# Kernel optimization log

Hardware: AMD Instinct MI355X
Metric: run time of the kernel (lower is better)

The kernel has to match this reference:

```python
import jax, jax.numpy as jnp
import numpy as np

N_NODES = 10000
N_EDGES = 160000
MUL = 128          # channel multiplicity
N_SPECIES = 10
SH_OFF = [0, 1, 4, 9, 16]   # spherical-harmonic offsets for l=0..3 (2l+1 each)
RADIAL_IN = 8
SIN_DIM = 32
MAX_DENSITY = 100.0


def setup_inputs() -> dict:
    key = jax.random.key(0)
    ks = jax.random.split(key, 16)
    inp = {
        'node_attrs': jax.random.normal(ks[0], (N_NODES, N_SPECIES), jnp.float32),
        'node_feats': jax.random.normal(ks[1], (N_NODES, MUL), jnp.float32),
        'edge_attrs': jax.random.normal(ks[2], (N_EDGES, 16), jnp.float32),
        'edge_feats': jax.random.normal(ks[3], (N_EDGES, RADIAL_IN), jnp.float32),
        'edge_index': jax.random.randint(ks[4], (2, N_EDGES), 0, N_NODES, jnp.int64),
        'W_up': jax.random.normal(ks[5], (MUL, MUL), jnp.float32),
        'Wr1': jax.random.normal(ks[6], (RADIAL_IN, 64), jnp.float32),
        'Wr2': jax.random.normal(ks[7], (64, 64), jnp.float32),
        'Wr3': jax.random.normal(ks[8], (64, 64), jnp.float32),
        'Wr4': jax.random.normal(ks[9], (64, 4 * MUL), jnp.float32),
        'Wd': jax.random.normal(ks[10], (RADIAL_IN, 1), jnp.float32),
        'Wsin': jax.random.normal(ks[11], (SIN_DIM, MUL), jnp.float32),
        'Wlin': jax.random.normal(ks[12], (4, MUL, MUL), jnp.float32),
        'Wskip': jax.random.normal(ks[13], (4, MUL, N_SPECIES, MUL), jnp.float32),
    }
    return inp


def _sinusoidal_embedding(x):
    # continuous sinusoidal embedding: dim=32, max_density=100
    half = SIN_DIM // 2
    freqs = jnp.exp(-jnp.log(MAX_DENSITY) * jnp.arange(half, dtype=x.dtype) / half)
    ang = x[:, None] * freqs[None, :]          # [N, 16]
    return jnp.concatenate([jnp.sin(ang), jnp.cos(ang)], axis=-1)  # [N, 32]


def reference(node_attrs, node_feats, edge_attrs, edge_feats, edge_index,
              W_up, Wr1, Wr2, Wr3, Wr4, Wd, Wsin, Wlin, Wskip):
    N = node_feats.shape[0]
    sender, receiver = edge_index[0], edge_index[1]

    # linear_up (e3nn o3.Linear on 128x0e, fan-in normalized)
    x = node_feats @ (W_up / np.float32(np.sqrt(MUL)))          # [N, 128]

    # radial MLP: FullyConnectedNet([8,64,64,64,512], silu), fan-in normalized
    h = edge_feats
    for W in (Wr1, Wr2, Wr3):
        h = jax.nn.silu(h @ (W / np.float32(np.sqrt(W.shape[0]))))
    tp_w = (h @ (Wr4 / np.float32(np.sqrt(64)))).reshape(-1, 4, MUL)  # [E, 4, 128]

    # equivariant TP: scalar node feats (x) gathered by sender, uvu path per SH l
    xs = x[sender]                                              # [E, 128]
    weighted = xs[:, None, :] * tp_w                            # [E, 4, 128]
    blocks = []
    for l in range(4):
        sh_l = edge_attrs[:, SH_OFF[l]:SH_OFF[l + 1]]           # [E, 2l+1]
        blk = weighted[:, l, :, None] * sh_l[:, None, :]        # [E, 128, 2l+1]
        blocks.append(blk.reshape(blk.shape[0], -1))
    mji = jnp.concatenate(blocks, axis=-1)                      # [E, 2048]

    # per-edge density gate
    density = jnp.tanh((edge_feats @ Wd) ** 2)                  # [E, 1]

    # scatter-sum messages and density to receivers
    message = jax.ops.segment_sum(mji, receiver, num_segments=N)        # [N, 2048]
    rho = jax.ops.segment_sum(density, receiver, num_segments=N)       # [N, 1]
    message = message / (rho + 1.0)

    # density embedding injected into the l=0 block
    demb = _sinusoidal_embedding(rho[:, 0]) @ Wsin              # [N, 128]
    message = message.at[:, :MUL].add(demb)

    # per-l linear (irreps_mid -> irreps_out), skip_tp with node_attrs, reshape
    out_blocks = []
    for l in range(4):
        d = 2 * l + 1
        blk = message[:, MUL * SH_OFF[l]:MUL * SH_OFF[l + 1]].reshape(N, MUL, d)
        blk = jnp.einsum('nuk,uv->nvk', blk, Wlin[l]) / np.float32(np.sqrt(MUL))
        blk = jnp.einsum('nvk,na,vaw->nwk', blk, node_attrs, Wskip[l]) \
              / np.float32(np.sqrt(MUL * N_SPECIES))
        out_blocks.append(blk)
    return jnp.concatenate(out_blocks, axis=-1)                 # [N, 128, 16]
```

## Files before the change

### kernel.cpp

```cpp
#include <hip/hip_runtime.h>
#include <hip/hip_bf16.h>

#define N_NODES 10000
#define N_EDGES 160000

typedef _Float16 h8 __attribute__((ext_vector_type(8)));
typedef _Float16 h4 __attribute__((ext_vector_type(4)));
typedef float f32x4 __attribute__((ext_vector_type(4)));

__device__ __forceinline__ float silu_f(float v){ return v / (1.f + expf(-v)); }

__global__ __launch_bounds__(256) void k_pre(const float* __restrict__ Wr2,
                                             const float* __restrict__ Wr3,
                                             const float* __restrict__ Wr4,
                                             const float* __restrict__ Wup,
                                             const float* __restrict__ Wlin,
                                             const float* __restrict__ Wskip,
                                             const int* __restrict__ eidx,
                                             _Float16* __restrict__ Wr2T,
                                             _Float16* __restrict__ Wr3T,
                                             _Float16* __restrict__ Wr4T,
                                             _Float16* __restrict__ WupT,
                                             _Float16* __restrict__ WC16T,
                                             int* __restrict__ cnt){
  const int b = blockIdx.x;
  __shared__ float wl[128];
  if (b < 224){
    const int idx = b*256 + threadIdx.x;
    if (idx < 4096){
      const int n = idx >> 6, k = idx & 63;
      Wr2T[idx] = (_Float16)(Wr2[k*64 + n] * 0.125f);
    } else if (idx < 8192){
      const int j = idx - 4096;
      const int n = j >> 6, k = j & 63;
      Wr3T[j] = (_Float16)(Wr3[k*64 + n] * 0.125f);
    } else if (idx < 40960){
      const int j = idx - 8192;
      const int n = j >> 6, k = j & 63;
      Wr4T[j] = (_Float16)(Wr4[k*512 + n] * 0.125f);
    } else if (idx < 57344){
      const int j = idx - 40960;
      const int u = j >> 7, k = j & 127;
      WupT[j] = (_Float16)(Wup[k*128 + u] * 0.08838834764831843f);
    }
  } else if (b < 736){
    const int lu = b - 224;
    const int l  = lu >> 7, u = lu & 127;
    if (threadIdx.x < 128) wl[threadIdx.x] = Wlin[lu*128 + threadIdx.x];
    __syncthreads();
    const float* Wsk = Wskip + (size_t)l * 163840;
    for (int i = threadIdx.x; i < 1280; i += 256){
      float acc = 0.f;
      #pragma unroll 16
      for (int v = 0; v < 128; ++v) acc += wl[v] * Wsk[v*1280 + i];
      const int a = i >> 7, w = i & 127;
      WC16T[((size_t)l*128 + w)*1280 + a*128 + u] =
          (_Float16)(acc * 0.0024705294220065465f);
    }
  } else {
    const int e = (b - 736)*256 + threadIdx.x;
    if (e < N_EDGES) atomicAdd(&cnt[eidx[N_EDGES + e]], 1);
  }
}

__global__ __launch_bounds__(256) void k_scan(const int* __restrict__ cnt,
                                              int* __restrict__ off,
                                              int* __restrict__ cur){
  __shared__ int sums[256];
  const int t = threadIdx.x;
  const int base = t * 40;
  int s = 0;
  for (int i = 0; i < 40; ++i){
    const int idx = base + i;
    if (idx < N_NODES) s += cnt[idx];
  }
  sums[t] = s;
  __syncthreads();
  for (int st = 1; st < 256; st <<= 1){
    const int v = (t >= st) ? sums[t - st] : 0;
    __syncthreads();
    sums[t] += v;
    __syncthreads();
  }
  int pre = (t > 0) ? sums[t - 1] : 0;
  for (int i = 0; i < 40; ++i){
    const int idx = base + i;
    if (idx < N_NODES){
      off[idx] = pre; cur[idx] = pre;
      pre += cnt[idx];
    }
  }
  if (t == 255) off[N_NODES] = sums[255];
}

__global__ __launch_bounds__(256) void k_mid(const int* __restrict__ eidx,
                                             int* __restrict__ cur,
                                             int* __restrict__ elist,
                                             int* __restrict__ esnd,
                                             const float* __restrict__ nf,
                                             const _Float16* __restrict__ WupT,
                                             float* __restrict__ x){
  const int b = blockIdx.x;
  const int tid = threadIdx.x;
  alignas(16) __shared__ _Float16 s_nf[64*128];
  alignas(16) __shared__ _Float16 s_wt[128*128];

  if (b < 625){
    const int e = b * 256 + tid;
    if (e < N_EDGES){
      const int pos = atomicAdd(&cur[eidx[N_EDGES + e]], 1);
      elist[pos] = e;
      esnd[pos]  = eidx[e];
    }
    return;
  }

  const int n0 = (b - 625) * 64;
  {
    const int rl = tid >> 2, part = tid & 3;
    const int gr = n0 + rl;
    #pragma unroll
    for (int j = 0; j < 4; ++j){
      const int cu = part*4 + j;
      h8 hv = (h8){};
      if (gr < N_NODES){
        const float4 v0 = *(const float4*)(nf + (size_t)gr*128 + cu*8);
        const float4 v1 = *(const float4*)(nf + (size_t)gr*128 + cu*8 + 4);
        hv[0]=(_Float16)v0.x; hv[1]=(_Float16)v0.y; hv[2]=(_Float16)v0.z; hv[3]=(_Float16)v0.w;
        hv[4]=(_Float16)v1.x; hv[5]=(_Float16)v1.y; hv[6]=(_Float16)v1.z; hv[7]=(_Float16)v1.w;
      }
      const int cs = (cu & 8) | ((cu & 7) ^ (rl & 7));
      *(h8*)&s_nf[rl*128 + cs*8] = hv;
    }
  }
  {
    const int rl = tid >> 1, part = tid & 1;
    #pragma unroll
    for (int j = 0; j < 8; ++j){
      const int cu = part*8 + j;
      const h8 v = *(const h8*)&WupT[(size_t)rl*128 + cu*8];
      const int cs = (cu & 8) | ((cu & 7) ^ (rl & 7));
      *(h8*)&s_wt[rl*128 + cs*8] = v;
    }
  }
  __syncthreads();

  const int wid = tid >> 6, lane = tid & 63;
  const int li = lane & 15, kg = lane >> 4;

  f32x4 acc[8];
  #pragma unroll
  for (int i = 0; i < 8; ++i) acc[i] = (f32x4){0,0,0,0};

  const int row = wid*16 + li;
  #pragma unroll
  for (int s = 0; s < 4; ++s){
    const int ca = s*4 + kg;
    const int csA = (ca & 8) | ((ca & 7) ^ (row & 7));
    const h8 af = *(const h8*)&s_nf[row*128 + csA*8];
    #pragma unroll
    for (int nt = 0; nt < 8; ++nt){
      const int u = nt*16 + li;
      const int csB = (ca & 8) | ((ca & 7) ^ (u & 7));
      const h8 bf = *(const h8*)&s_wt[u*128 + csB*8];
      acc[nt] = __builtin_amdgcn_mfma_f32_16x16x32_f16(af, bf, acc[nt], 0, 0, 0);
    }
  }
  #pragma unroll
  for (int nt = 0; nt < 8; ++nt){
    #pragma unroll
    for (int r = 0; r < 4; ++r){
      const int gr = n0 + wid*16 + kg*4 + r;
      if (gr < N_NODES) x[(size_t)gr*128 + nt*16 + li] = acc[nt][r];
    }
  }
}

__global__ __launch_bounds__(256) void k_fused(const float* __restrict__ ef,
                                               const float* __restrict__ ea,
                                               const float* __restrict__ x,
                                               const float* __restrict__ Wr1,
                                               const float* __restrict__ Wd,
                                               const _Float16* __restrict__ Wr2T,
                                               const _Float16* __restrict__ Wr3T,
                                               const _Float16* __restrict__ Wr4T,
                                               const float* __restrict__ Wsin,
                                               const int* __restrict__ off,
                                               const int* __restrict__ elist,
                                               const int* __restrict__ esnd,
                                               float* __restrict__ msg){
  const int n0 = blockIdx.x * 4;
  const int tid = threadIdx.x;
  const int lane = tid & 63, wid = tid >> 6;
  const int li = lane & 15, kg = lane >> 4;
  const int u = tid & 127, h = tid >> 7;

  __shared__ int   s_eid[32];
  __shared__ float s_ef[32][8];
  __shared__ float s_w1[8][64];
  alignas(16) __shared__ _Float16 s_xs[32][136];
  alignas(16) __shared__ _Float16 s_actA[32][64];
  alignas(16) __shared__ _Float16 s_actB[32][64];
  alignas(16) __shared__ _Float16 s_w2[32][520];
  alignas(16) __shared__ float s_sh[32][16];
  __shared__ float s_dd[32];
  __shared__ float s_rho[4];
  __shared__ int   s_offs[5];
  __shared__ float s_emb[4][32];

  if (tid < 5) s_offs[tid] = off[n0 + tid];
  if (tid < 4) s_rho[tid] = 0.f;
  for (int j = tid; j < 512; j += 256) s_w1[j >> 6][j & 63] = Wr1[j];
  __syncthreads();

  const int beg = s_offs[0], end = s_offs[4];
  const int ngrp = (end - beg + 31) >> 5;

  float a0[8] = {0,0,0,0,0,0,0,0};
  float a1[8] = {0,0,0,0,0,0,0,0};
  float a2[8] = {0,0,0,0,0,0,0,0};
  float a3[8] = {0,0,0,0,0,0,0,0};

  for (int grp = 0; grp < ngrp; ++grp){
    const int pbase = beg + grp*32;

    if (tid < 32) s_eid[tid] = (pbase + tid < end) ? elist[pbase + tid] : -1;
    __syncthreads();

    {
      const int e = tid >> 3, i = tid & 7;
      const int eid = s_eid[e];
      s_ef[e][i] = (eid >= 0) ? ef[(size_t)eid*8 + i] : 0.f;
    }
    {
      const int e = tid >> 3, qq = tid & 7;
      const int p = pbase + e;
      const int snd = (p < end) ? esnd[p] : 0;
      const float4* xp = (const float4*)(x + (size_t)snd*128 + qq*16);
      #pragma unroll
      for (int j = 0; j < 4; ++j){
        const float4 v = xp[j];
        h4 hv; hv[0]=(_Float16)v.x; hv[1]=(_Float16)v.y; hv[2]=(_Float16)v.z; hv[3]=(_Float16)v.w;
        *(h4*)&s_xs[e][qq*16 + j*4] = hv;
      }
    }
    #pragma unroll
    for (int c2 = 0; c2 < 2; ++c2){
      const int idx = c2*256 + tid;
      const int slot = idx >> 4, jj = idx & 15;
      const int eid = s_eid[slot];
      s_sh[slot][jj] = (eid >= 0) ? ea[(size_t)eid*16 + jj] : 0.f;
    }
    __syncthreads();

    if (tid < 32){
      float s = 0.f;
      #pragma unroll
      for (int i = 0; i < 8; ++i) s += s_ef[tid][i] * Wd[i];
      s_dd[tid] = tanhf(s*s);
    }

    {
      const int e = tid >> 3, ng = tid & 7;
      float hv[8] = {0,0,0,0,0,0,0,0};
      #pragma unroll
      for (int k = 0; k < 8; ++k){
        const float ev = s_ef[e][k] * 0.3535533905932738f;
        #pragma unroll
        for (int j = 0; j < 8; ++j) hv[j] += ev * s_w1[k][ng*8 + j];
      }
      h8 o;
      #pragma unroll
      for (int j = 0; j < 8; ++j) o[j] = (_Float16)silu_f(hv[j]);
      *(h8*)&s_actA[e][(ng ^ (e & 7))*8] = o;
    }
    __syncthreads();

    {
      h8 af[2];
      #pragma unroll
      for (int s = 0; s < 2; ++s)
        af[s] = *(const h8*)&Wr2T[(size_t)(wid*16 + li)*64 + s*32 + kg*8];
      #pragma unroll
      for (int nt = 0; nt < 2; ++nt){
        const int e = nt*16 + li;
        f32x4 acc = (f32x4){0,0,0,0};
        #pragma unroll
        for (int s = 0; s < 2; ++s){
          const h8 bf = *(const h8*)&s_actA[e][((s*4 + kg) ^ (e & 7))*8];
          acc = __builtin_amdgcn_mfma_f32_16x16x32_f16(af[s], bf, acc, 0, 0, 0);
        }
        #pragma unroll
        for (int r = 0; r < 4; ++r){
          const int n = wid*16 + kg*4 + r;
          s_actB[e][((n >> 3) ^ (e & 7))*8 + (n & 7)] = (_Float16)silu_f(acc[r]);
        }
      }
    }
    __syncthreads();

    {
      h8 af[2];
      #pragma unroll
      for (int s = 0; s < 2; ++s)
        af[s] = *(const h8*)&Wr3T[(size_t)(wid*16 + li)*64 + s*32 + kg*8];
      #pragma unroll
      for (int nt = 0; nt < 2; ++nt){
        const int e = nt*16 + li;
        f32x4 acc = (f32x4){0,0,0,0};
        #pragma unroll
        for (int s = 0; s < 2; ++s){
          const h8 bf = *(const h8*)&s_actB[e][((s*4 + kg) ^ (e & 7))*8];
          acc = __builtin_amdgcn_mfma_f32_16x16x32_f16(af[s], bf, acc, 0, 0, 0);
        }
        #pragma unroll
        for (int r = 0; r < 4; ++r){
          const int n = wid*16 + kg*4 + r;
          s_actA[e][((n >> 3) ^ (e & 7))*8 + (n & 7)] = (_Float16)silu_f(acc[r]);
        }
      }
    }
    __syncthreads();

    {
      h8 bf[2][2];
      #pragma unroll
      for (int nt = 0; nt < 2; ++nt){
        const int e = nt*16 + li;
        #pragma unroll
        for (int s = 0; s < 2; ++s)
          bf[nt][s] = *(const h8*)&s_actA[e][((s*4 + kg) ^ (e & 7))*8];
      }
      #pragma unroll
      for (int p = 0; p < 2; ++p){
        #pragma unroll
        for (int mt = 0; mt < 4; ++mt){
          const int nbase = wid*128 + p*64 + mt*16;
          h8 af[2];
          #pragma unroll
          for (int s = 0; s < 2; ++s)
            af[s] = *(const h8*)&Wr4T[(size_t)(nbase + li)*64 + s*32 + kg*8];
          f32x4 acc[2];
          #pragma unroll
          for (int nt = 0; nt < 2; ++nt){
            acc[nt] = (f32x4){0,0,0,0};
            #pragma unroll
            for (int s = 0; s < 2; ++s)
              acc[nt] = __builtin_amdgcn_mfma_f32_16x16x32_f16(af[s], bf[nt][s], acc[nt], 0, 0, 0);
          }
          const int c0 = nbase + kg*4;
          const int u0 = c0 & 127;
          #pragma unroll
          for (int nt = 0; nt < 2; ++nt){
            const int e = nt*16 + li;
            const h4 xv = *(const h4*)&s_xs[e][u0];
            h4 ov;
            #pragma unroll
            for (int r = 0; r < 4; ++r) ov[r] = (_Float16)acc[nt][r] * xv[r];
            *(h4*)&s_w2[e][c0] = ov;
          }
        }
      }
    }
    __syncthreads();

    int lo0 = s_offs[0] - pbase; lo0 = lo0 < 0 ? 0 : lo0;
    int hi0 = s_offs[1] - pbase; hi0 = hi0 > 32 ? 32 : (hi0 < 0 ? 0 : hi0);
    int lo1 = s_offs[1] - pbase; lo1 = lo1 < 0 ? 0 : lo1;
    int hi1 = s_offs[2] - pbase; hi1 = hi1 > 32 ? 32 : (hi1 < 0 ? 0 : hi1);
    int lo2 = s_offs[2] - pbase; lo2 = lo2 < 0 ? 0 : lo2;
    int hi2 = s_offs[3] - pbase; hi2 = hi2 > 32 ? 32 : (hi2 < 0 ? 0 : hi2);
    int lo3 = s_offs[3] - pbase; lo3 = lo3 < 0 ? 0 : lo3;
    int hi3 = s_offs[4] - pbase; hi3 = hi3 > 32 ? 32 : (hi3 < 0 ? 0 : hi3);

#define ACC_H0(A, LO, HI)                                            \
    for (int s = (LO); s < (HI); ++s){                               \
      const float wa  = (float)s_w2[s][u];                           \
      const float wb  = (float)s_w2[s][128 + u];                     \
      const float wcv = (float)s_w2[s][256 + u];                     \
      const float4 sa = *(const float4*)&s_sh[s][0];                 \
      const float4 sb = *(const float4*)&s_sh[s][4];                 \
      A[0] += wa*sa.x;                                               \
      A[1] += wb*sa.y;  A[2] += wb*sa.z;  A[3] += wb*sa.w;           \
      A[4] += wcv*sb.x; A[5] += wcv*sb.y;                            \
      A[6] += wcv*sb.z; A[7] += wcv*sb.w;                            \
    }
#define ACC_H1(A, LO, HI)                                            \
    for (int s = (LO); s < (HI); ++s){                               \
      const float wcv = (float)s_w2[s][256 + u];                     \
      const float wd  = (float)s_w2[s][384 + u];                     \
      const float4 sa = *(const float4*)&s_sh[s][8];                 \
      const float4 sb = *(const float4*)&s_sh[s][12];                \
      A[0] += wcv*sa.x;                                              \
      A[1] += wd*sa.y;  A[2] += wd*sa.z;  A[3] += wd*sa.w;           \
      A[4] += wd*sb.x;  A[5] += wd*sb.y;                             \
      A[6] += wd*sb.z;  A[7] += wd*sb.w;                             \
    }

    if (h == 0){
      ACC_H0(a0, lo0, hi0) ACC_H0(a1, lo1, hi1)
      ACC_H0(a2, lo2, hi2) ACC_H0(a3, lo3, hi3)
    } else {
      ACC_H1(a0, lo0, hi0) ACC_H1(a1, lo1, hi1)
      ACC_H1(a2, lo2, hi2) ACC_H1(a3, lo3, hi3)
    }

    if (tid < 4){
      int lo = s_offs[tid]     - pbase; lo = lo < 0 ? 0 : lo;
      int hi = s_offs[tid + 1] - pbase; hi = hi > 32 ? 32 : (hi < 0 ? 0 : hi);
      float r = 0.f;
      for (int s = lo; s < hi; ++s) r += s_dd[s];
      s_rho[tid] += r;
    }
    __syncthreads();
  }

  if (tid < 64){
    const int ni = tid >> 4, f = tid & 15;
    const float fr  = expf(-0.28782313662425572f * (float)f);
    const float ang = s_rho[ni] * fr;
    s_emb[ni][f]      = sinf(ang);
    s_emb[ni][f + 16] = cosf(ang);
  }
  __syncthreads();

  float db0 = 0.f, db1 = 0.f, db2 = 0.f, db3 = 0.f;
  if (h == 0){
    #pragma unroll 8
    for (int j = 0; j < 32; ++j){
      const float wsv = Wsin[j*128 + u];
      db0 += s_emb[0][j]*wsv; db1 += s_emb[1][j]*wsv;
      db2 += s_emb[2][j]*wsv; db3 += s_emb[3][j]*wsv;
    }
  }
  const float t0 = 1.f/(s_rho[0]+1.f), t1 = 1.f/(s_rho[1]+1.f);
  const float t2 = 1.f/(s_rho[2]+1.f), t3 = 1.f/(s_rho[3]+1.f);
  #pragma unroll
  for (int j = 0; j < 8; ++j){
    float v0 = a0[j]*t0, v1 = a1[j]*t1, v2 = a2[j]*t2, v3 = a3[j]*t3;
    if (h == 0 && j == 0){ v0 += db0; v1 += db1; v2 += db2; v3 += db3; }
    const size_t base = (size_t)(h*8 + j)*128 + u;
    msg[(size_t)(n0+0)*2048 + base] = v0;
    msg[(size_t)(n0+1)*2048 + base] = v1;
    msg[(size_t)(n0+2)*2048 + base] = v2;
    msg[(size_t)(n0+3)*2048 + base] = v3;
  }
}

template<int L, int D>
__device__ __forceinline__ void final_body(const int bb,
                                           const float* __restrict__ msg,
                                           const float* __restrict__ attrs,
                                           const _Float16* __restrict__ WC16T,
                                           float* __restrict__ outD,
                                           _Float16* __restrict__ sA,
                                           _Float16* __restrict__ sB,
                                           _Float16* __restrict__ sAttr){
  constexpr int OFF  = (L==0 ? 0 : L==1 ? 1 : L==2 ? 4 : 9);
  constexpr int ROWS = N_NODES * D;
  const int r0  = bb * 128;
  const int tid = threadIdx.x;

  {
    const int rl = tid >> 2, quarter = tid & 3;
    const int gr = r0 + rl;
    h8 vals[4];
    if (gr < ROWS){
      const int n = gr / D, k = gr - n*D;
      const float4* src = (const float4*)(msg + (size_t)n*2048 + (size_t)(OFF+k)*128 + quarter*32);
      #pragma unroll
      for (int j = 0; j < 4; ++j){
        const float4 v0 = src[j*2], v1 = src[j*2+1];
        h8 hv;
        hv[0]=(_Float16)v0.x; hv[1]=(_Float16)v0.y; hv[2]=(_Float16)v0.z; hv[3]=(_Float16)v0.w;
        hv[4]=(_Float16)v1.x; hv[5]=(_Float16)v1.y; hv[6]=(_Float16)v1.z; hv[7]=(_Float16)v1.w;
        vals[j] = hv;
      }
    } else {
      #pragma unroll
      for (int j = 0; j < 4; ++j) vals[j] = (h8){};
    }
    #pragma unroll
    for (int j = 0; j < 4; ++j){
      const int cu = quarter*4 + j;
      const int cs = (cu & 8) | ((cu & 7) ^ (rl & 7));
      *(h8*)&sA[rl*128 + cs*8] = vals[j];
    }
  }
  for (int i = tid; i < 1280; i += 512){
    const int rl = i / 10, aa = i - rl*10;
    const int gr = r0 + rl;
    sAttr[i] = (gr < ROWS) ? (_Float16)attrs[(gr / D)*10 + aa] : (_Float16)0.f;
  }
  {
    const int w = tid >> 2, part = tid & 3;
    const _Float16* src = WC16T + ((size_t)L*128 + w)*1280 + part*16;
    #pragma unroll
    for (int j = 0; j < 2; ++j){
      const h8 v = *(const h8*)(src + j*8);
      const int cc = part*2 + j;
      *(h8*)&sB[w*64 + (cc ^ (w & 7))*8] = v;
    }
  }
  __syncthreads();

  const int wid = tid >> 6, lane = tid & 63;
  const int wm = wid >> 2, wn = wid & 3;
  const int li = lane & 15, kg = lane >> 4;

  f32x4 acc[4][2];
  #pragma unroll
  for (int m = 0; m < 4; ++m)
    #pragma unroll
    for (int nn = 0; nn < 2; ++nn) acc[m][nn] = (f32x4){0,0,0,0};

  for (int step = 0; step < 20; ++step){
    _Float16* sbc = (step & 1) ? (sB + 8192) : sB;
    _Float16* sbn = (step & 1) ? sB : (sB + 8192);
    const bool more = (step + 1 < 20);
    h8 pre[2];
    if (more){
      const int a2 = (step+1) >> 1, u02 = ((step+1) & 1) << 6;
      const _Float16* src = WC16T + ((size_t)L*128 + (tid>>2))*1280 + a2*128 + u02 + (tid&3)*16;
      #pragma unroll
      for (int j = 0; j < 2; ++j) pre[j] = *(const h8*)(src + j*8);
    }

    const int a  = step >> 1;
    const int uh = (step & 1) << 3;

    h8 afr[4][2], bfr[2][2];
    #pragma unroll
    for (int m = 0; m < 4; ++m){
      const int row = wm*64 + m*16 + li;
      const _Float16 av = sAttr[row*10 + a];
      h8 avx;
      #pragma unroll
      for (int j = 0; j < 8; ++j) avx[j] = av;
      #pragma unroll
      for (int s = 0; s < 2; ++s){
        const int ca = uh + s*4 + kg;
        const int cs = (ca & 8) | ((ca & 7) ^ (row & 7));
        const h8 mA = *(const h8*)&sA[row*128 + cs*8];
        afr[m][s] = mA * avx;
      }
    }
    #pragma unroll
    for (int nn = 0; nn < 2; ++nn){
      const int w = wn*32 + nn*16 + li;
      #pragma unroll
      for (int s = 0; s < 2; ++s){
        const int cb = s*4 + kg;
        bfr[nn][s] = *(const h8*)&sbc[w*64 + ((cb ^ (w & 7)))*8];
      }
    }
    #pragma unroll
    for (int s = 0; s < 2; ++s)
      #pragma unroll
      for (int m = 0; m < 4; ++m)
        #pragma unroll
        for (int nn = 0; nn < 2; ++nn)
          acc[m][nn] = __builtin_amdgcn_mfma_f32_16x16x32_f16(afr[m][s], bfr[nn][s], acc[m][nn], 0, 0, 0);

    if (more){
      const int w = tid >> 2, part = tid & 3;
      #pragma unroll
      for (int j = 0; j < 2; ++j){
        const int cc = part*2 + j;
        *(h8*)&sbn[w*64 + (cc ^ (w & 7))*8] = pre[j];
      }
    }
    __syncthreads();
  }

  #pragma unroll
  for (int m = 0; m < 4; ++m){
    const int rbase = r0 + wm*64 + m*16 + kg*4;
    #pragma unroll
    for (int rr = 0; rr < 4; ++rr){
      const int gr = rbase + rr;
      if (gr < ROWS){
        float* op = outD + (size_t)gr*128;
        #pragma unroll
        for (int nn = 0; nn < 2; ++nn)
          op[wn*32 + nn*16 + li] = acc[m][nn][rr];
      }
    }
  }
}

__global__ __launch_bounds__(512) void k_final_all(const float* __restrict__ msg,
                                                   const float* __restrict__ attrs,
                                                   const _Float16* __restrict__ WC16T,
                                                   float* __restrict__ outD){
  alignas(16) __shared__ _Float16 sA[128*128];
  alignas(16) __shared__ _Float16 sB[2*64*128];
  __shared__ _Float16 sAttr[128*10];
  const int b = blockIdx.x;
  if (b < 79)       final_body<0,1>(b,       msg, attrs, WC16T, outD,            sA, sB, sAttr);
  else if (b < 314) final_body<1,3>(b - 79,  msg, attrs, WC16T, outD + 1280000,  sA, sB, sAttr);
  else if (b < 705) final_body<2,5>(b - 314, msg, attrs, WC16T, outD + 5120000,  sA, sB, sAttr);
  else              final_body<3,7>(b - 705, msg, attrs, WC16T, outD + 11520000, sA, sB, sAttr);
}

__global__ __launch_bounds__(256) void k_merge(const float* __restrict__ outD,
                                               float* __restrict__ out){
  const int n0 = blockIdx.x * 4;
  const int tid = threadIdx.x;
  __shared__ float lds[4*16*132];

  {
    const float4* src = (const float4*)(outD + (size_t)n0*128);
    for (int j = tid; j < 128; j += 256){
      const int row = j >> 5, c4 = j & 31;
      *(float4*)&lds[(row*16 + 0)*132 + c4*4] = src[j];
    }
  }
  {
    const float4* src = (const float4*)(outD + 1280000 + (size_t)n0*3*128);
    for (int j = tid; j < 384; j += 256){
      const int row = j >> 5, c4 = j & 31;
      const int nloc = row/3, k = row - nloc*3;
      *(float4*)&lds[(nloc*16 + 1 + k)*132 + c4*4] = src[j];
    }
  }
  {
    const float4* src = (const float4*)(outD + 5120000 + (size_t)n0*5*128);
    for (int j = tid; j < 640; j += 256){
      const int row = j >> 5, c4 = j & 31;
      const int nloc = row/5, k = row - nloc*5;
      *(float4*)&lds[(nloc*16 + 4 + k)*132 + c4*4] = src[j];
    }
  }
  {
    const float4* src = (const float4*)(outD + 11520000 + (size_t)n0*7*128);
    for (int j = tid; j < 896; j += 256){
      const int row = j >> 5, c4 = j & 31;
      const int nloc = row/7, k = row - nloc*7;
      *(float4*)&lds[(nloc*16 + 9 + k)*132 + c4*4] = src[j];
    }
  }
  __syncthreads();

  for (int j = tid; j < 2048; j += 256){
    const int nloc = j >> 9, qv = j & 511;
    const int w = qv >> 2, s0 = (qv & 3) << 2;
    float4 v;
    v.x = lds[(nloc*16 + s0 + 0)*132 + w];
    v.y = lds[(nloc*16 + s0 + 1)*132 + w];
    v.z = lds[(nloc*16 + s0 + 2)*132 + w];
    v.w = lds[(nloc*16 + s0 + 3)*132 + w];
    *(float4*)&out[(size_t)(n0 + nloc)*2048 + qv*4] = v;
  }
}

extern "C" void kernel_launch(void* const* d_in, const int* in_sizes, int n_in,
                              void* d_out, int out_size, void* d_ws, size_t ws_size,
                              hipStream_t stream){
  const float* node_attrs = (const float*)d_in[0];
  const float* node_feats = (const float*)d_in[1];
  const float* edge_attrs = (const float*)d_in[2];
  const float* edge_feats = (const float*)d_in[3];
  const int*   edge_index = (const int*)d_in[4];
  const float* W_up  = (const float*)d_in[5];
  const float* Wr1   = (const float*)d_in[6];
  const float* Wr2   = (const float*)d_in[7];
  const float* Wr3   = (const float*)d_in[8];
  const float* Wr4   = (const float*)d_in[9];
  const float* Wd    = (const float*)d_in[10];
  const float* Wsin  = (const float*)d_in[11];
  const float* Wlin  = (const float*)d_in[12];
  const float* Wskip = (const float*)d_in[13];
  float* out = (float*)d_out;

  float* outD    = (float*)d_ws;
  float* msg     = outD + 20480000;
  float* x       = msg + 20480000;
  _Float16* WC16T= (_Float16*)(x + 1280000);
  int* cnt   = (int*)(WC16T + 655360);
  int* off   = cnt + 10000;
  int* cur   = off + 10016;
  int* elist = cur + 10000;
  int* esnd  = elist + 160000;
  _Float16* Wr2T = (_Float16*)(esnd + 160000);
  _Float16* Wr3T = Wr2T + 4096;
  _Float16* Wr4T = Wr3T + 4096;
  _Float16* WupT = Wr4T + 32768;

  hipMemsetAsync(cnt, 0, (size_t)10000 * sizeof(int), stream);

  k_pre<<<1361, 256, 0, stream>>>(Wr2, Wr3, Wr4, W_up, Wlin, Wskip, edge_index,
                                  Wr2T, Wr3T, Wr4T, WupT, WC16T, cnt);
  k_scan<<<1, 256, 0, stream>>>(cnt, off, cur);
  k_mid<<<782, 256, 0, stream>>>(edge_index, cur, elist, esnd,
                                 node_feats, WupT, x);

  k_fused<<<N_NODES/4, 256, 0, stream>>>(edge_feats, edge_attrs, x,
                                         Wr1, Wd, Wr2T, Wr3T, Wr4T, Wsin,
                                         off, elist, esnd, msg);

  k_final_all<<<1252, 512, 0, stream>>>(msg, node_attrs, WC16T, outD);

  k_merge<<<2500, 256, 0, stream>>>(outD, out);
}
```

Baseline: 335.6 us.

## Store messages in fp16, fuse final per-l GEMMs with output merge, split Wr4 pass

The fused edge kernel now builds the Wr4 weights in two passes over a half-width LDS buffer and accumulates between them, which shrinks shared memory per block. It writes the message as fp16 instead of fp32. A new final kernel processes 16 nodes per block across all four l blocks. It writes output directly in the interleaved [N,128,16] layout, so the separate per-l output buffer and merge kernel are gone. This removes an fp32 round trip through global memory and one launch, but adds an extra barrier per edge group and keeps the message at fp16 precision.

```diff
diff --git a/kernel.cpp b/kernel.cpp
--- a/kernel.cpp
+++ b/kernel.cpp
@@ -188,7 +188,7 @@
                                                const int* __restrict__ off,
                                                const int* __restrict__ elist,
                                                const int* __restrict__ esnd,
-                                               float* __restrict__ msg){
+                                               _Float16* __restrict__ msg16){
   const int n0 = blockIdx.x * 4;
   const int tid = threadIdx.x;
   const int lane = tid & 63, wid = tid >> 6;
@@ -198,10 +198,10 @@
   __shared__ int   s_eid[32];
   __shared__ float s_ef[32][8];
   __shared__ float s_w1[8][64];
-  alignas(16) __shared__ _Float16 s_xs[32][136];
+  alignas(16) __shared__ _Float16 s_xs[32][132];
   alignas(16) __shared__ _Float16 s_actA[32][64];
   alignas(16) __shared__ _Float16 s_actB[32][64];
-  alignas(16) __shared__ _Float16 s_w2[32][520];
+  alignas(16) __shared__ _Float16 s_w2[32][264];
   alignas(16) __shared__ float s_sh[32][16];
   __shared__ float s_dd[32];
   __shared__ float s_rho[4];
@@ -317,48 +317,6 @@
         for (int r = 0; r < 4; ++r){
           const int n = wid*16 + kg*4 + r;
           s_actA[e][((n >> 3) ^ (e & 7))*8 + (n & 7)] = (_Float16)silu_f(acc[r]);
-        }
-      }
-    }
-    __syncthreads();
-
-    {
-      h8 bf[2][2];
-      #pragma unroll
-      for (int nt = 0; nt < 2; ++nt){
-        const int e = nt*16 + li;
-        #pragma unroll
-        for (int s = 0; s < 2; ++s)
-          bf[nt][s] = *(const h8*)&s_actA[e][((s*4 + kg) ^ (e & 7))*8];
-      }
-      #pragma unroll
-      for (int p = 0; p < 2; ++p){
-        #pragma unroll
-        for (int mt = 0; mt < 4; ++mt){
-          const int nbase = wid*128 + p*64 + mt*16;
-          h8 af[2];
-          #pragma unroll
-          for (int s = 0; s < 2; ++s)
-            af[s] = *(const h8*)&Wr4T[(size_t)(nbase + li)*64 + s*32 + kg*8];
-          f32x4 acc[2];
-          #pragma unroll
-          for (int nt = 0; nt < 2; ++nt){
-            acc[nt] = (f32x4){0,0,0,0};
-            #pragma unroll
-            for (int s = 0; s < 2; ++s)
-              acc[nt] = __builtin_amdgcn_mfma_f32_16x16x32_f16(af[s], bf[nt][s], acc[nt], 0, 0, 0);
-          }
-          const int c0 = nbase + kg*4;
-          const int u0 = c0 & 127;
-          #pragma unroll
-          for (int nt = 0; nt < 2; ++nt){
-            const int e = nt*16 + li;
-            const h4 xv = *(const h4*)&s_xs[e][u0];
-            h4 ov;
-            #pragma unroll
-            for (int r = 0; r < 4; ++r) ov[r] = (_Float16)acc[nt][r] * xv[r];
-            *(h4*)&s_w2[e][c0] = ov;
-          }
         }
       }
     }
@@ -373,22 +331,34 @@
     int lo3 = s_offs[3] - pbase; lo3 = lo3 < 0 ? 0 : lo3;
     int hi3 = s_offs[4] - pbase; hi3 = hi3 > 32 ? 32 : (hi3 < 0 ? 0 : hi3);
 
-#define ACC_H0(A, LO, HI)                                            \
+    h8 bf[2][2];
+    #pragma unroll
+    for (int nt = 0; nt < 2; ++nt){
+      const int e = nt*16 + li;
+      #pragma unroll
+      for (int s = 0; s < 2; ++s)
+        bf[nt][s] = *(const h8*)&s_actA[e][((s*4 + kg) ^ (e & 7))*8];
+    }
+
+#define ACCA(A, LO, HI)                                              \
     for (int s = (LO); s < (HI); ++s){                               \
       const float wa  = (float)s_w2[s][u];                           \
       const float wb  = (float)s_w2[s][128 + u];                     \
-      const float wcv = (float)s_w2[s][256 + u];                     \
       const float4 sa = *(const float4*)&s_sh[s][0];                 \
-      const float4 sb = *(const float4*)&s_sh[s][4];                 \
       A[0] += wa*sa.x;                                               \
       A[1] += wb*sa.y;  A[2] += wb*sa.z;  A[3] += wb*sa.w;           \
+    }
+#define ACCB0(A, LO, HI)                                             \
+    for (int s = (LO); s < (HI); ++s){                               \
+      const float wcv = (float)s_w2[s][u];                           \
+      const float4 sb = *(const float4*)&s_sh[s][4];                 \
       A[4] += wcv*sb.x; A[5] += wcv*sb.y;                            \
       A[6] += wcv*sb.z; A[7] += wcv*sb.w;                            \
     }
-#define ACC_H1(A, LO, HI)                                            \
+#define ACCB1(A, LO, HI)                                             \
     for (int s = (LO); s < (HI); ++s){                               \
-      const float wcv = (float)s_w2[s][256 + u];                     \
-      const float wd  = (float)s_w2[s][384 + u];                     \
+      const float wcv = (float)s_w2[s][u];                           \
+      const float wd  = (float)s_w2[s][128 + u];                     \
       const float4 sa = *(const float4*)&s_sh[s][8];                 \
       const float4 sb = *(const float4*)&s_sh[s][12];                \
       A[0] += wcv*sa.x;                                              \
@@ -397,22 +367,61 @@
       A[6] += wd*sb.z;  A[7] += wd*sb.w;                             \
     }
 
-    if (h == 0){
-      ACC_H0(a0, lo0, hi0) ACC_H0(a1, lo1, hi1)
-      ACC_H0(a2, lo2, hi2) ACC_H0(a3, lo3, hi3)
-    } else {
-      ACC_H1(a0, lo0, hi0) ACC_H1(a1, lo1, hi1)
-      ACC_H1(a2, lo2, hi2) ACC_H1(a3, lo3, hi3)
-    }
-
-    if (tid < 4){
-      int lo = s_offs[tid]     - pbase; lo = lo < 0 ? 0 : lo;
-      int hi = s_offs[tid + 1] - pbase; hi = hi > 32 ? 32 : (hi < 0 ? 0 : hi);
-      float r = 0.f;
-      for (int s = lo; s < hi; ++s) r += s_dd[s];
-      s_rho[tid] += r;
-    }
-    __syncthreads();
+    #pragma unroll
+    for (int pass = 0; pass < 2; ++pass){
+      #pragma unroll
+      for (int mt = 0; mt < 4; ++mt){
+        const int cc0 = wid*64 + mt*16;
+        const int nb  = pass*256 + cc0;
+        h8 af[2];
+        #pragma unroll
+        for (int s = 0; s < 2; ++s)
+          af[s] = *(const h8*)&Wr4T[(size_t)(nb + li)*64 + s*32 + kg*8];
+        f32x4 acc[2];
+        #pragma unroll
+        for (int nt = 0; nt < 2; ++nt){
+          acc[nt] = (f32x4){0,0,0,0};
+          #pragma unroll
+          for (int s = 0; s < 2; ++s)
+            acc[nt] = __builtin_amdgcn_mfma_f32_16x16x32_f16(af[s], bf[nt][s], acc[nt], 0, 0, 0);
+        }
+        const int cc = cc0 + kg*4;
+        const int u0 = cc & 127;
+        #pragma unroll
+        for (int nt = 0; nt < 2; ++nt){
+          const int e = nt*16 + li;
+          const h4 xv = *(const h4*)&s_xs[e][u0];
+          h4 ov;
+          #pragma unroll
+          for (int r = 0; r < 4; ++r) ov[r] = (_Float16)acc[nt][r] * xv[r];
+          *(h4*)&s_w2[e][cc] = ov;
+        }
+      }
+      __syncthreads();
+
+      if (pass == 0){
+        if (h == 0){
+          ACCA(a0, lo0, hi0) ACCA(a1, lo1, hi1)
+          ACCA(a2, lo2, hi2) ACCA(a3, lo3, hi3)
+        }
+      } else {
+        if (h == 0){
+          ACCB0(a0, lo0, hi0) ACCB0(a1, lo1, hi1)
+          ACCB0(a2, lo2, hi2) ACCB0(a3, lo3, hi3)
+        } else {
+          ACCB1(a0, lo0, hi0) ACCB1(a1, lo1, hi1)
+          ACCB1(a2, lo2, hi2) ACCB1(a3, lo3, hi3)
+        }
+        if (tid < 4){
+          int lo = s_offs[tid]     - pbase; lo = lo < 0 ? 0 : lo;
+          int hi = s_offs[tid + 1] - pbase; hi = hi > 32 ? 32 : (hi < 0 ? 0 : hi);
+          float r = 0.f;
+          for (int s = lo; s < hi; ++s) r += s_dd[s];
+          s_rho[tid] += r;
+        }
+      }
+      __syncthreads();
+    }
   }
 
   if (tid < 64){
@@ -440,217 +449,108 @@
     float v0 = a0[j]*t0, v1 = a1[j]*t1, v2 = a2[j]*t2, v3 = a3[j]*t3;
     if (h == 0 && j == 0){ v0 += db0; v1 += db1; v2 += db2; v3 += db3; }
     const size_t base = (size_t)(h*8 + j)*128 + u;
-    msg[(size_t)(n0+0)*2048 + base] = v0;
-    msg[(size_t)(n0+1)*2048 + base] = v1;
-    msg[(size_t)(n0+2)*2048 + base] = v2;
-    msg[(size_t)(n0+3)*2048 + base] = v3;
+    msg16[(size_t)(n0+0)*2048 + base] = (_Float16)v0;
+    msg16[(size_t)(n0+1)*2048 + base] = (_Float16)v1;
+    msg16[(size_t)(n0+2)*2048 + base] = (_Float16)v2;
+    msg16[(size_t)(n0+3)*2048 + base] = (_Float16)v3;
   }
 }
 
-template<int L, int D>
-__device__ __forceinline__ void final_body(const int bb,
-                                           const float* __restrict__ msg,
-                                           const float* __restrict__ attrs,
-                                           const _Float16* __restrict__ WC16T,
-                                           float* __restrict__ outD,
-                                           _Float16* __restrict__ sA,
-                                           _Float16* __restrict__ sB,
-                                           _Float16* __restrict__ sAttr){
-  constexpr int OFF  = (L==0 ? 0 : L==1 ? 1 : L==2 ? 4 : 9);
-  constexpr int ROWS = N_NODES * D;
-  const int r0  = bb * 128;
+__global__ __launch_bounds__(512) void k_final16(const _Float16* __restrict__ msg16,
+                                                 const float* __restrict__ attrs,
+                                                 const _Float16* __restrict__ WC16T,
+                                                 float* __restrict__ out){
+  const int n0 = blockIdx.x * 16;
   const int tid = threadIdx.x;
 
+  alignas(16) __shared__ _Float16 msgh[16*2048];
+  alignas(16) __shared__ _Float16 Bh[2][4*128*36];
+  __shared__ _Float16 attrh[160];
+
   {
-    const int rl = tid >> 2, quarter = tid & 3;
-    const int gr = r0 + rl;
-    h8 vals[4];
-    if (gr < ROWS){
-      const int n = gr / D, k = gr - n*D;
-      const float4* src = (const float4*)(msg + (size_t)n*2048 + (size_t)(OFF+k)*128 + quarter*32);
-      #pragma unroll
-      for (int j = 0; j < 4; ++j){
-        const float4 v0 = src[j*2], v1 = src[j*2+1];
-        h8 hv;
-        hv[0]=(_Float16)v0.x; hv[1]=(_Float16)v0.y; hv[2]=(_Float16)v0.z; hv[3]=(_Float16)v0.w;
-        hv[4]=(_Float16)v1.x; hv[5]=(_Float16)v1.y; hv[6]=(_Float16)v1.z; hv[7]=(_Float16)v1.w;
-        vals[j] = hv;
-      }
-    } else {
-      #pragma unroll
-      for (int j = 0; j < 4; ++j) vals[j] = (h8){};
-    }
-    #pragma unroll
-    for (int j = 0; j < 4; ++j){
-      const int cu = quarter*4 + j;
-      const int cs = (cu & 8) | ((cu & 7) ^ (rl & 7));
-      *(h8*)&sA[rl*128 + cs*8] = vals[j];
-    }
-  }
-  for (int i = tid; i < 1280; i += 512){
-    const int rl = i / 10, aa = i - rl*10;
-    const int gr = r0 + rl;
-    sAttr[i] = (gr < ROWS) ? (_Float16)attrs[(gr / D)*10 + aa] : (_Float16)0.f;
-  }
+    const int node = tid >> 5, s5 = tid & 31;
+    const int sk = s5 >> 1, half = s5 & 1;
+    const _Float16* src = msg16 + (size_t)(n0 + node)*2048 + sk*128 + half*64;
+    #pragma unroll
+    for (int j = 0; j < 8; ++j){
+      const h8 v = *(const h8*)(src + j*8);
+      const int cu = half*8 + j;
+      const int cs = (cu & 8) | ((cu & 7) ^ (node & 7));
+      *(h8*)&msgh[node*2048 + sk*128 + cs*8] = v;
+    }
+  }
+  if (tid < 160) attrh[tid] = (_Float16)attrs[n0*10 + tid];
   {
-    const int w = tid >> 2, part = tid & 3;
-    const _Float16* src = WC16T + ((size_t)L*128 + w)*1280 + part*16;
-    #pragma unroll
-    for (int j = 0; j < 2; ++j){
-      const h8 v = *(const h8*)(src + j*8);
-      const int cc = part*2 + j;
-      *(h8*)&sB[w*64 + (cc ^ (w & 7))*8] = v;
-    }
+    const int l = tid >> 7, w = tid & 127;
+    const _Float16* src = WC16T + ((size_t)l*128 + w)*1280;
+    #pragma unroll
+    for (int c = 0; c < 4; ++c)
+      *(h8*)&Bh[0][l*4608 + w*36 + c*8] = *(const h8*)(src + c*8);
   }
   __syncthreads();
 
   const int wid = tid >> 6, lane = tid & 63;
-  const int wm = wid >> 2, wn = wid & 3;
   const int li = lane & 15, kg = lane >> 4;
-
-  f32x4 acc[4][2];
+  const int wcol = wid*16 + li;
+
+  f32x4 acc[16];
   #pragma unroll
-  for (int m = 0; m < 4; ++m)
-    #pragma unroll
-    for (int nn = 0; nn < 2; ++nn) acc[m][nn] = (f32x4){0,0,0,0};
-
-  for (int step = 0; step < 20; ++step){
-    _Float16* sbc = (step & 1) ? (sB + 8192) : sB;
-    _Float16* sbn = (step & 1) ? sB : (sB + 8192);
-    const bool more = (step + 1 < 20);
-    h8 pre[2];
+  for (int i = 0; i < 16; ++i) acc[i] = (f32x4){0,0,0,0};
+
+  for (int step = 0; step < 40; ++step){
+    const _Float16* bc = &Bh[step & 1][0];
+    _Float16* bn = &Bh[(step & 1) ^ 1][0];
+    const bool more = (step + 1 < 40);
+    h8 pre[4];
     if (more){
-      const int a2 = (step+1) >> 1, u02 = ((step+1) & 1) << 6;
-      const _Float16* src = WC16T + ((size_t)L*128 + (tid>>2))*1280 + a2*128 + u02 + (tid&3)*16;
-      #pragma unroll
-      for (int j = 0; j < 2; ++j) pre[j] = *(const h8*)(src + j*8);
-    }
-
-    const int a  = step >> 1;
-    const int uh = (step & 1) << 3;
-
-    h8 afr[4][2], bfr[2][2];
-    #pragma unroll
-    for (int m = 0; m < 4; ++m){
-      const int row = wm*64 + m*16 + li;
-      const _Float16 av = sAttr[row*10 + a];
-      h8 avx;
-      #pragma unroll
-      for (int j = 0; j < 8; ++j) avx[j] = av;
-      #pragma unroll
-      for (int s = 0; s < 2; ++s){
-        const int ca = uh + s*4 + kg;
-        const int cs = (ca & 8) | ((ca & 7) ^ (row & 7));
-        const h8 mA = *(const h8*)&sA[row*128 + cs*8];
-        afr[m][s] = mA * avx;
-      }
-    }
-    #pragma unroll
-    for (int nn = 0; nn < 2; ++nn){
-      const int w = wn*32 + nn*16 + li;
-      #pragma unroll
-      for (int s = 0; s < 2; ++s){
-        const int cb = s*4 + kg;
-        bfr[nn][s] = *(const h8*)&sbc[w*64 + ((cb ^ (w & 7)))*8];
-      }
-    }
-    #pragma unroll
-    for (int s = 0; s < 2; ++s)
-      #pragma unroll
-      for (int m = 0; m < 4; ++m)
-        #pragma unroll
-        for (int nn = 0; nn < 2; ++nn)
-          acc[m][nn] = __builtin_amdgcn_mfma_f32_16x16x32_f16(afr[m][s], bfr[nn][s], acc[m][nn], 0, 0, 0);
+      const int a2 = (step + 1) >> 2, u02 = ((step + 1) & 3) * 32;
+      const int l = tid >> 7, w = tid & 127;
+      const _Float16* src = WC16T + ((size_t)l*128 + w)*1280 + a2*128 + u02;
+      #pragma unroll
+      for (int c = 0; c < 4; ++c) pre[c] = *(const h8*)(src + c*8);
+    }
+
+    const int a  = step >> 2;
+    const int ca = (step & 3)*4 + kg;
+    const int cs = (ca & 8) | ((ca & 7) ^ (li & 7));
+    const _Float16 av = attrh[li*10 + a];
+    h8 avx;
+    #pragma unroll
+    for (int j = 0; j < 8; ++j) avx[j] = av;
+
+    h8 bfr[4];
+    #pragma unroll
+    for (int l = 0; l < 4; ++l)
+      bfr[l] = *(const h8*)&bc[l*4608 + wcol*36 + kg*8];
+
+    #pragma unroll
+    for (int sk = 0; sk < 16; ++sk){
+      const int lm = (sk == 0) ? 0 : (sk < 4) ? 1 : (sk < 9) ? 2 : 3;
+      const h8 mA = *(const h8*)&msgh[li*2048 + sk*128 + cs*8];
+      acc[sk] = __builtin_amdgcn_mfma_f32_16x16x32_f16(mA * avx, bfr[lm], acc[sk], 0, 0, 0);
+    }
 
     if (more){
-      const int w = tid >> 2, part = tid & 3;
-      #pragma unroll
-      for (int j = 0; j < 2; ++j){
-        const int cc = part*2 + j;
-        *(h8*)&sbn[w*64 + (cc ^ (w & 7))*8] = pre[j];
-      }
+      const int l = tid >> 7, w = tid & 127;
+      #pragma unroll
+      for (int c = 0; c < 4; ++c)
+        *(h8*)&bn[l*4608 + w*36 + c*8] = pre[c];
     }
     __syncthreads();
   }
 
   #pragma unroll
-  for (int m = 0; m < 4; ++m){
-    const int rbase = r0 + wm*64 + m*16 + kg*4;
-    #pragma unroll
-    for (int rr = 0; rr < 4; ++rr){
-      const int gr = rbase + rr;
-      if (gr < ROWS){
-        float* op = outD + (size_t)gr*128;
-        #pragma unroll
-        for (int nn = 0; nn < 2; ++nn)
-          op[wn*32 + nn*16 + li] = acc[m][nn][rr];
-      }
-    }
-  }
-}
-
-__global__ __launch_bounds__(512) void k_final_all(const float* __restrict__ msg,
-                                                   const float* __restrict__ attrs,
-                                                   const _Float16* __restrict__ WC16T,
-                                                   float* __restrict__ outD){
-  alignas(16) __shared__ _Float16 sA[128*128];
-  alignas(16) __shared__ _Float16 sB[2*64*128];
-  __shared__ _Float16 sAttr[128*10];
-  const int b = blockIdx.x;
-  if (b < 79)       final_body<0,1>(b,       msg, attrs, WC16T, outD,            sA, sB, sAttr);
-  else if (b < 314) final_body<1,3>(b - 79,  msg, attrs, WC16T, outD + 1280000,  sA, sB, sAttr);
-  else if (b < 705) final_body<2,5>(b - 314, msg, attrs, WC16T, outD + 5120000,  sA, sB, sAttr);
-  else              final_body<3,7>(b - 705, msg, attrs, WC16T, outD + 11520000, sA, sB, sAttr);
-}
-
-__global__ __launch_bounds__(256) void k_merge(const float* __restrict__ outD,
-                                               float* __restrict__ out){
-  const int n0 = blockIdx.x * 4;
-  const int tid = threadIdx.x;
-  __shared__ float lds[4*16*132];
-
-  {
-    const float4* src = (const float4*)(outD + (size_t)n0*128);
-    for (int j = tid; j < 128; j += 256){
-      const int row = j >> 5, c4 = j & 31;
-      *(float4*)&lds[(row*16 + 0)*132 + c4*4] = src[j];
-    }
-  }
-  {
-    const float4* src = (const float4*)(outD + 1280000 + (size_t)n0*3*128);
-    for (int j = tid; j < 384; j += 256){
-      const int row = j >> 5, c4 = j & 31;
-      const int nloc = row/3, k = row - nloc*3;
-      *(float4*)&lds[(nloc*16 + 1 + k)*132 + c4*4] = src[j];
-    }
-  }
-  {
-    const float4* src = (const float4*)(outD + 5120000 + (size_t)n0*5*128);
-    for (int j = tid; j < 640; j += 256){
-      const int row = j >> 5, c4 = j & 31;
-      const int nloc = row/5, k = row - nloc*5;
-      *(float4*)&lds[(nloc*16 + 4 + k)*132 + c4*4] = src[j];
-    }
-  }
-  {
-    const float4* src = (const float4*)(outD + 11520000 + (size_t)n0*7*128);
-    for (int j = tid; j < 896; j += 256){
-      const int row = j >> 5, c4 = j & 31;
-      const int nloc = row/7, k = row - nloc*7;
-      *(float4*)&lds[(nloc*16 + 9 + k)*132 + c4*4] = src[j];
-    }
-  }
-  __syncthreads();
-
-  for (int j = tid; j < 2048; j += 256){
-    const int nloc = j >> 9, qv = j & 511;
-    const int w = qv >> 2, s0 = (qv & 3) << 2;
-    float4 v;
-    v.x = lds[(nloc*16 + s0 + 0)*132 + w];
-    v.y = lds[(nloc*16 + s0 + 1)*132 + w];
-    v.z = lds[(nloc*16 + s0 + 2)*132 + w];
-    v.w = lds[(nloc*16 + s0 + 3)*132 + w];
-    *(float4*)&out[(size_t)(n0 + nloc)*2048 + qv*4] = v;
+  for (int r = 0; r < 4; ++r){
+    const int node = kg*4 + r;
+    float* op = out + (size_t)(n0 + node)*2048 + wcol*16;
+    float4 v0 = {acc[0][r],  acc[1][r],  acc[2][r],  acc[3][r]};
+    float4 v1 = {acc[4][r],  acc[5][r],  acc[6][r],  acc[7][r]};
+    float4 v2 = {acc[8][r],  acc[9][r],  acc[10][r], acc[11][r]};
+    float4 v3 = {acc[12][r], acc[13][r], acc[14][r], acc[15][r]};
+    *(float4*)(op)      = v0;
+    *(float4*)(op + 4)  = v1;
+    *(float4*)(op + 8)  = v2;
+    *(float4*)(op + 12) = v3;
   }
 }
 
@@ -673,10 +573,9 @@
   const float* Wskip = (const float*)d_in[13];
   float* out = (float*)d_out;
 
-  float* outD    = (float*)d_ws;
-  float* msg     = outD + 20480000;
-  float* x       = msg + 20480000;
-  _Float16* WC16T= (_Float16*)(x + 1280000);
+  _Float16* msg16 = (_Float16*)d_ws;
+  float* x        = (float*)(msg16 + 20480000);
+  _Float16* WC16T = (_Float16*)(x + 1280000);
   int* cnt   = (int*)(WC16T + 655360);
   int* off   = cnt + 10000;
   int* cur   = off + 10016;
@@ -697,9 +596,7 @@
 
   k_fused<<<N_NODES/4, 256, 0, stream>>>(edge_feats, edge_attrs, x,
                                          Wr1, Wd, Wr2T, Wr3T, Wr4T, Wsin,
-                                         off, elist, esnd, msg);
-
-  k_final_all<<<1252, 512, 0, stream>>>(msg, node_attrs, WC16T, outD);
-
-  k_merge<<<2500, 256, 0, stream>>>(outD, out);
+                                         off, elist, esnd, msg16);
+
+  k_final16<<<N_NODES/16, 512, 0, stream>>>(msg16, node_attrs, WC16T, out);
 }
```

Measured after the change: 561.4 us. +67.3%, slower.
